# Kernel tuning notes

Measured on AMD Instinct MI355X. Metric: run time of the kernel, lower is better.

## Reference

```python
import jax, jax.numpy as jnp
import numpy as np

N_HEADS = 16
N_EMB = 1024
HEAD_SIZE = 64
BLOCK_SIZE = 2048


def setup_inputs() -> dict:
    key = jax.random.key(0)
    k1, k2, k3, k4, k5 = jax.random.split(key, 5)
    B, T, E, H, D = 4, BLOCK_SIZE, N_EMB, N_HEADS, HEAD_SIZE
    s = 1.0 / np.sqrt(E)
    x = jax.random.normal(k1, (B, T, E), dtype=jnp.float32)
    # Stacked per-head projection weights (Linear with bias=False): [H, E, D]
    Wq = jax.random.normal(k2, (H, E, D), dtype=jnp.float32) * s
    Wk = jax.random.normal(k3, (H, E, D), dtype=jnp.float32) * s
    Wv = jax.random.normal(k4, (H, E, D), dtype=jnp.float32) * s
    Wo = jax.random.normal(k5, (H * D, E), dtype=jnp.float32) * (1.0 / np.sqrt(H * D))
    return {"x": x, "Wq": Wq, "Wk": Wk, "Wv": Wv, "Wo": Wo}


def reference(x, Wq, Wk, Wv, Wo):
    # x: [B,T,E]; Wq/Wk/Wv: [H,E,D]; Wo: [H*D,E]
    B, T, E = x.shape
    H, _, D = Wq.shape
    q = jnp.einsum('bte,hed->bhtd', x, Wq)
    k = jnp.einsum('bte,hed->bhtd', x, Wk)
    v = jnp.einsum('bte,hed->bhtd', x, Wv)
    scores = jnp.einsum('bhtd,bhsd->bhts', q, k) * (D ** -0.5)  # [B,H,T,T]
    causal = jnp.tril(jnp.ones((T, T), dtype=bool))
    scores = jnp.where(causal, scores, -jnp.inf)
    wei = jax.nn.softmax(scores, axis=-1)  # dropout is identity in eval mode
    out = jnp.einsum('bhts,bhsd->bhtd', wei, v)  # [B,H,T,D]
    out = out.transpose(0, 2, 1, 3).reshape(B, T, H * D)  # concat heads
    return out @ Wo  # [B,T,E]
```

## Files before the change

### kernel.cpp

```cpp
#include <hip/hip_runtime.h>

#define B_  4
#define T_  2048
#define E_  1024
#define H_  16
#define D_  64
#define HD_ 1024
#define BT_ 8192

typedef __bf16 bf16x8 __attribute__((ext_vector_type(8)));
typedef float  f32x4  __attribute__((ext_vector_type(4)));

static __device__ __forceinline__ unsigned short f2bf(float f) {
  __bf16 h = (__bf16)f;
  return __builtin_bit_cast(unsigned short, h);
}
static __device__ __forceinline__ bf16x8 ldb8(const unsigned short* p) {
  return *(const bf16x8*)p;
}

#define GLD_LDS16(gp, lp)                                                      \
  __builtin_amdgcn_global_load_lds(                                            \
      (const __attribute__((address_space(1))) void*)(gp),                     \
      (__attribute__((address_space(3))) void*)(lp), 16, 0, 0)

__global__ __launch_bounds__(256) void prep_k(const float* __restrict__ x,
                                              const float* __restrict__ Wq,
                                              const float* __restrict__ Wk,
                                              const float* __restrict__ Wv,
                                              const float* __restrict__ Wo,
                                              unsigned short* __restrict__ xb,
                                              unsigned short* __restrict__ wT,
                                              unsigned short* __restrict__ woT) {
  const int bid = blockIdx.x, tid = threadIdx.x;
  if (bid < 2048) {
    #pragma unroll
    for (int p = 0; p < 4; ++p) {
      int i = bid * 1024 + p * 256 + tid;
      float4 v = ((const float4*)x)[i];
      ushort4 o;
      o.x = f2bf(v.x); o.y = f2bf(v.y); o.z = f2bf(v.z); o.w = f2bf(v.w);
      ((ushort4*)xb)[i] = o;
    }
    return;
  }
  __shared__ float tl[64 * 65];
  if (bid < 2816) {
    const int tix = bid - 2048;
    const int w = tix >> 8;
    const int h = (tix >> 4) & 15;
    const int e0 = (tix & 15) * 64;
    const float* src = (w == 0) ? Wq : (w == 1) ? Wk : Wv;
    #pragma unroll
    for (int rr = 0; rr < 4; ++rr) {
      const int e = e0 + rr * 16 + (tid >> 4);
      const int d4 = (tid & 15) * 4;
      float4 v = *(const float4*)&src[(size_t)(h * 1024 + e) * 64 + d4];
      tl[(e - e0) * 65 + d4 + 0] = v.x;
      tl[(e - e0) * 65 + d4 + 1] = v.y;
      tl[(e - e0) * 65 + d4 + 2] = v.z;
      tl[(e - e0) * 65 + d4 + 3] = v.w;
    }
    __syncthreads();
    #pragma unroll
    for (int cc = 0; cc < 4; ++cc) {
      const int d = cc * 16 + (tid >> 4);
      const int e4 = (tid & 15) * 4;
      ushort4 o;
      o.x = f2bf(tl[(e4 + 0) * 65 + d]);
      o.y = f2bf(tl[(e4 + 1) * 65 + d]);
      o.z = f2bf(tl[(e4 + 2) * 65 + d]);
      o.w = f2bf(tl[(e4 + 3) * 65 + d]);
      *(ushort4*)&wT[(size_t)((w * 16 + h) * 64 + d) * 1024 + e0 + e4] = o;
    }
    return;
  }
  {
    const int tix = bid - 2816;
    const int hd0 = (tix >> 4) * 64;
    const int e0 = (tix & 15) * 64;
    #pragma unroll
    for (int rr = 0; rr < 4; ++rr) {
      const int hd = hd0 + rr * 16 + (tid >> 4);
      const int e4 = (tid & 15) * 4;
      float4 v = *(const float4*)&Wo[(size_t)hd * 1024 + e0 + e4];
      tl[(hd - hd0) * 65 + e4 + 0] = v.x;
      tl[(hd - hd0) * 65 + e4 + 1] = v.y;
      tl[(hd - hd0) * 65 + e4 + 2] = v.z;
      tl[(hd - hd0) * 65 + e4 + 3] = v.w;
    }
    __syncthreads();
    #pragma unroll
    for (int cc = 0; cc < 4; ++cc) {
      const int e = e0 + cc * 16 + (tid >> 4);
      const int hd4 = (tid & 15) * 4;
      ushort4 o;
      o.x = f2bf(tl[(hd4 + 0) * 65 + (e - e0)]);
      o.y = f2bf(tl[(hd4 + 1) * 65 + (e - e0)]);
      o.z = f2bf(tl[(hd4 + 2) * 65 + (e - e0)]);
      o.w = f2bf(tl[(hd4 + 3) * 65 + (e - e0)]);
      *(ushort4*)&woT[(size_t)e * 1024 + hd0 + hd4] = o;
    }
  }
}

static __device__ __forceinline__ void gemm_core(const unsigned short* __restrict__ A,
                                                 const unsigned short* __restrict__ BT,
                                                 const int K, const int m0, const int n0,
                                                 unsigned short* lA, unsigned short* lB,
                                                 f32x4 acc[4][4]) {
  const int tid  = threadIdx.x;
  const int wave = tid >> 6;
  const int lane = tid & 63;
  const int wm = wave & 1, wn = wave >> 1;
  const int l16 = lane & 15, quad = lane >> 4;
  const int nkt = K >> 6;

  const int sr = tid >> 3;
  const int sc = ((tid & 7) ^ (sr & 7)) * 8;
  const int sw = l16 & 7;
  const int sl0 = (quad ^ sw) << 3;
  const int sl1 = ((4 + quad) ^ sw) << 3;

#define STG(kt) do {                                                            \
    const size_t kb = (size_t)(kt) * 64 + sc;                                   \
    unsigned short* dA = lA + ((kt) & 1) * 8192 + wave * 512;                   \
    unsigned short* dB = lB + ((kt) & 1) * 8192 + wave * 512;                   \
    GLD_LDS16(A  + (size_t)(m0 +      sr) * K + kb, dA);                        \
    GLD_LDS16(A  + (size_t)(m0 + 32 + sr) * K + kb, dA + 2048);                 \
    GLD_LDS16(A  + (size_t)(m0 + 64 + sr) * K + kb, dA + 4096);                 \
    GLD_LDS16(A  + (size_t)(m0 + 96 + sr) * K + kb, dA + 6144);                 \
    GLD_LDS16(BT + (size_t)(n0 +      sr) * K + kb, dB);                        \
    GLD_LDS16(BT + (size_t)(n0 + 32 + sr) * K + kb, dB + 2048);                 \
    GLD_LDS16(BT + (size_t)(n0 + 64 + sr) * K + kb, dB + 4096);                 \
    GLD_LDS16(BT + (size_t)(n0 + 96 + sr) * K + kb, dB + 6144);                 \
  } while (0)

  #pragma unroll
  for (int i = 0; i < 4; ++i)
    #pragma unroll
    for (int j = 0; j < 4; ++j) acc[i][j] = (f32x4){0.f, 0.f, 0.f, 0.f};

  STG(0);
  for (int kt = 0; kt < nkt; ++kt) {
    __syncthreads();
    if (kt + 1 < nkt) STG(kt + 1);
    const unsigned short* cA = lA + (kt & 1) * 8192;
    const unsigned short* cB = lB + (kt & 1) * 8192;
    bf16x8 aF[4][2], bF[4][2];
    #pragma unroll
    for (int mi = 0; mi < 4; ++mi) {
      const int ar = (wm * 64 + mi * 16 + l16) * 64;
      aF[mi][0] = ldb8(cA + ar + sl0);
      aF[mi][1] = ldb8(cA + ar + sl1);
    }
    #pragma unroll
    for (int nj = 0; nj < 4; ++nj) {
      const int br = (wn * 64 + nj * 16 + l16) * 64;
      bF[nj][0] = ldb8(cB + br + sl0);
      bF[nj][1] = ldb8(cB + br + sl1);
    }
    __builtin_amdgcn_s_setprio(1);
    #pragma unroll
    for (int mi = 0; mi < 4; ++mi)
      #pragma unroll
      for (int nj = 0; nj < 4; ++nj) {
        acc[mi][nj] = __builtin_amdgcn_mfma_f32_16x16x32_bf16(aF[mi][0], bF[nj][0],
                                                              acc[mi][nj], 0, 0, 0);
        acc[mi][nj] = __builtin_amdgcn_mfma_f32_16x16x32_bf16(aF[mi][1], bF[nj][1],
                                                              acc[mi][nj], 0, 0, 0);
      }
    __builtin_amdgcn_s_setprio(0);
  }
#undef STG
}

__global__ __launch_bounds__(256) void qkv_gemm_k(const unsigned short* __restrict__ xb,
                                                  const unsigned short* __restrict__ wT,
                                                  unsigned short* __restrict__ q,
                                                  unsigned short* __restrict__ k,
                                                  unsigned short* __restrict__ vT) {
  __shared__ unsigned short lA[2 * 128 * 64], lB[2 * 128 * 64];
  f32x4 acc[4][4];
  const int m0 = blockIdx.x * 128, n0 = blockIdx.y * 128;
  gemm_core(xb, wT, E_, m0, n0, lA, lB, acc);

  const int wave = threadIdx.x >> 6, lane = threadIdx.x & 63;
  const int wm = wave & 1, wn = wave >> 1;
  const int l16 = lane & 15, quad = lane >> 4;
  const int type = n0 >> 10;
  const float C = 0.18033688011112042f;
  #pragma unroll
  for (int i = 0; i < 4; ++i) {
    #pragma unroll
    for (int j = 0; j < 4; ++j) {
      const int n = n0 + wn * 64 + j * 16 + l16;
      const int h = (n >> 6) & 15, d = n & 63;
      #pragma unroll
      for (int r = 0; r < 4; ++r) {
        const int m = m0 + wm * 64 + i * 16 + quad * 4 + r;
        const int b = m >> 11, t = m & (T_ - 1);
        if (type == 0)
          q[((size_t)(b * H_ + h) * T_ + t) * D_ + d] = f2bf(acc[i][j][r] * C);
        else if (type == 1)
          k[((size_t)(b * H_ + h) * T_ + t) * D_ + d] = f2bf(acc[i][j][r]);
        else
          vT[((size_t)(b * H_ + h) * D_ + d) * T_ + t] = f2bf(acc[i][j][r]);
      }
    }
  }
}

__global__ __launch_bounds__(256) void proj_k(const unsigned short* __restrict__ ao,
                                              const unsigned short* __restrict__ woT,
                                              float* __restrict__ out) {
  __shared__ unsigned short lA[2 * 128 * 64], lB[2 * 128 * 64];
  f32x4 acc[4][4];
  const int m0 = blockIdx.x * 128, n0 = blockIdx.y * 128;
  gemm_core(ao, woT, HD_, m0, n0, lA, lB, acc);

  const int wave = threadIdx.x >> 6, lane = threadIdx.x & 63;
  const int wm = wave & 1, wn = wave >> 1;
  const int l16 = lane & 15, quad = lane >> 4;
  #pragma unroll
  for (int i = 0; i < 4; ++i)
    #pragma unroll
    for (int j = 0; j < 4; ++j)
      #pragma unroll
      for (int r = 0; r < 4; ++r)
        out[(size_t)(m0 + wm * 64 + i * 16 + quad * 4 + r) * E_ +
            n0 + wn * 64 + j * 16 + l16] = acc[i][j][r];
}

__global__ __launch_bounds__(256) void attn_k(const unsigned short* __restrict__ q,
                                              const unsigned short* __restrict__ k,
                                              const unsigned short* __restrict__ vT,
                                              unsigned short* __restrict__ ao) {
  __shared__ unsigned short lK[2][64 * 64];
  __shared__ unsigned short lV[2][64 * 64];
  __shared__ unsigned short lP[4][32][72];
  const int tid  = threadIdx.x;
  const int lane = tid & 63;
  const int wave = tid >> 6;
  const int l16  = lane & 15;
  const int quad = lane >> 4;
  const int id    = (int)blockIdx.x;
  const int bhid  = id & 63;
  const int qpair = id >> 6;
  const int h = bhid & 15, b = bhid >> 4;
  const size_t bh = (size_t)(b * H_ + h);
  const unsigned short* qp = q  + bh * (T_ * D_);
  const unsigned short* kp = k  + bh * (T_ * D_);
  const unsigned short* vp = vT + bh * (D_ * T_);

  const int srow = tid >> 3;
  const int kseg = (tid & 7) ^ (srow & 7);
  const int sw = (l16 & 7);

  #pragma unroll
  for (int pr = 0; pr < 2; ++pr) {
    const int qblk = (pr == 0) ? qpair : 15 - qpair;
    const int q0 = qblk * 128 + wave * 32;

    bf16x8 aq[2][2];
    #pragma unroll
    for (int rb = 0; rb < 2; ++rb)
      #pragma unroll
      for (int hh = 0; hh < 2; ++hh)
        aq[rb][hh] = ldb8(qp + (q0 + rb * 16 + l16) * D_ + hh * 32 + quad * 8);

    float lr[2][4];
    f32x4 o[2][4];
    #pragma unroll
    for (int rb = 0; rb < 2; ++rb) {
      #pragma unroll
      for (int r = 0; r < 4; ++r) lr[rb][r] = 0.f;
      #pragma unroll
      for (int nb = 0; nb < 4; ++nb) o[rb][nb] = (f32x4){0.f, 0.f, 0.f, 0.f};
    }

    const int nch = 2 * (qblk + 1);

    {
      unsigned short* Kb = lK[0];
      unsigned short* Vb = lV[0];
      GLD_LDS16(kp + srow * D_ + kseg * 8, Kb + wave * 512);
      GLD_LDS16(kp + (32 + srow) * D_ + kseg * 8, Kb + 2048 + wave * 512);
      GLD_LDS16(vp + (size_t)srow * T_ + kseg * 8, Vb + wave * 512);
      GLD_LDS16(vp + (size_t)(32 + srow) * T_ + kseg * 8, Vb + 2048 + wave * 512);
    }

    for (int c = 0; c < nch; ++c) {
      __syncthreads();
      if (c + 1 < nch) {
        const int s1 = (c + 1) * 64;
        unsigned short* Kb = lK[(c + 1) & 1];
        unsigned short* Vb = lV[(c + 1) & 1];
        GLD_LDS16(kp + (s1 + srow) * D_ + kseg * 8, Kb + wave * 512);
        GLD_LDS16(kp + (s1 + 32 + srow) * D_ + kseg * 8, Kb + 2048 + wave * 512);
        GLD_LDS16(vp + (size_t)srow * T_ + s1 + kseg * 8, Vb + wave * 512);
        GLD_LDS16(vp + (size_t)(32 + srow) * T_ + s1 + kseg * 8, Vb + 2048 + wave * 512);
      }
      const int s0 = c * 64;
      const unsigned short* Kb = lK[c & 1];
      const unsigned short* Vb = lV[c & 1];
      f32x4 sc[2][4];
      #pragma unroll
      for (int rb = 0; rb < 2; ++rb)
        #pragma unroll
        for (int j = 0; j < 4; ++j) sc[rb][j] = (f32x4){0.f, 0.f, 0.f, 0.f};
      #pragma unroll
      for (int j = 0; j < 4; ++j) {
        const int sr = j * 16 + l16;
        bf16x8 bk0 = ldb8(Kb + sr * 64 + ((quad ^ sw) << 3));
        bf16x8 bk1 = ldb8(Kb + sr * 64 + (((4 + quad) ^ sw) << 3));
        #pragma unroll
        for (int rb = 0; rb < 2; ++rb) {
          sc[rb][j] = __builtin_amdgcn_mfma_f32_16x16x32_bf16(aq[rb][0], bk0, sc[rb][j], 0, 0, 0);
          sc[rb][j] = __builtin_amdgcn_mfma_f32_16x16x32_bf16(aq[rb][1], bk1, sc[rb][j], 0, 0, 0);
        }
      }
      const bool domask = (c == nch - 1) || (c == nch - 2);
      #pragma unroll
      for (int rb = 0; rb < 2; ++rb) {
        #pragma unroll
        for (int j = 0; j < 4; ++j) {
          #pragma unroll
          for (int r = 0; r < 4; ++r) {
            float p = __builtin_amdgcn_exp2f(sc[rb][j][r]);
            if (domask) {
              const int qg = q0 + rb * 16 + quad * 4 + r;
              if (s0 + j * 16 + l16 > qg) p = 0.f;
            }
            lr[rb][r] += p;
            lP[wave][rb * 16 + quad * 4 + r][j * 16 + l16] = f2bf(p);
          }
        }
      }
      __builtin_amdgcn_wave_barrier();
      bf16x8 aP[2][2];
      #pragma unroll
      for (int rb = 0; rb < 2; ++rb)
        #pragma unroll
        for (int hh = 0; hh < 2; ++hh)
          aP[rb][hh] = ldb8(&lP[wave][rb * 16 + l16][hh * 32 + quad * 8]);
      __builtin_amdgcn_wave_barrier();
      #pragma unroll
      for (int nb = 0; nb < 4; ++nb) {
        const int d = nb * 16 + l16;
        bf16x8 bV0 = ldb8(Vb + d * 64 + ((quad ^ sw) << 3));
        bf16x8 bV1 = ldb8(Vb + d * 64 + (((4 + quad) ^ sw) << 3));
        #pragma unroll
        for (int rb = 0; rb < 2; ++rb) {
          o[rb][nb] = __builtin_amdgcn_mfma_f32_16x16x32_bf16(aP[rb][0], bV0, o[rb][nb], 0, 0, 0);
          o[rb][nb] = __builtin_amdgcn_mfma_f32_16x16x32_bf16(aP[rb][1], bV1, o[rb][nb], 0, 0, 0);
        }
      }
    }

    #pragma unroll
    for (int off = 1; off < 16; off <<= 1)
      #pragma unroll
      for (int rb = 0; rb < 2; ++rb)
        #pragma unroll
        for (int r = 0; r < 4; ++r)
          lr[rb][r] += __shfl_xor(lr[rb][r], off, 64);
    #pragma unroll
    for (int rb = 0; rb < 2; ++rb) {
      #pragma unroll
      for (int r = 0; r < 4; ++r) {
        const float inv = 1.0f / lr[rb][r];
        const int t = q0 + rb * 16 + quad * 4 + r;
        #pragma unroll
        for (int nb = 0; nb < 4; ++nb)
          ao[((size_t)(b * T_ + t) * H_ + h) * D_ + nb * 16 + l16] = f2bf(o[rb][nb][r] * inv);
      }
    }
  }
}


extern "C" void kernel_launch(void* const* d_in, const int* in_sizes, int n_in,
                              void* d_out, int out_size, void* d_ws, size_t ws_size,
                              hipStream_t stream) {
  const float* x  = (const float*)d_in[0];
  const float* Wq = (const float*)d_in[1];
  const float* Wk = (const float*)d_in[2];
  const float* Wv = (const float*)d_in[3];
  const float* Wo = (const float*)d_in[4];
  float* out = (float*)d_out;

  char* ws = (char*)d_ws;
  unsigned short* xb   = (unsigned short*)(ws + 0);
  unsigned short* wT   = (unsigned short*)(ws + 16777216);
  unsigned short* woT  = (unsigned short*)(ws + 23068672);
  unsigned short* qb   = (unsigned short*)(ws + 25165824);
  unsigned short* kb   = (unsigned short*)(ws + 41943040);
  unsigned short* vTb  = (unsigned short*)(ws + 58720256);
  unsigned short* aob  = (unsigned short*)(ws + 75497472);

  prep_k<<<dim3(3072), dim3(256), 0, stream>>>(x, Wq, Wk, Wv, Wo, xb, wT, woT);
  qkv_gemm_k<<<dim3(BT_ / 128, 3072 / 128), dim3(256), 0, stream>>>(xb, wT, qb, kb, vTb);
  attn_k<<<dim3(512), dim3(256), 0, stream>>>(qb, kb, vTb, aob);
  proj_k<<<dim3(BT_ / 128, E_ / 128), dim3(256), 0, stream>>>(aob, woT, out);
}
```

Measured before the change: 252.8 us.

## Use triple-buffered K=32 pipeline with vmcnt waits for QKV GEMM

Adds a new GEMM core for the QKV projection that uses K-tiles of 32 with three LDS buffers, issuing loads two iterations ahead. Explicit vmcnt waits plus raw barriers replace the full __syncthreads. The goal is to hide global-to-LDS latency better and shrink LDS usage from 64KB to 48KB, which may allow higher occupancy. In exchange it doubles the number of loop iterations and barriers per K. The output projection keeps the original double-buffered K=64 core.

```diff
diff --git a/kernel.cpp b/kernel.cpp
--- a/kernel.cpp
+++ b/kernel.cpp
@@ -104,11 +104,80 @@
   }
 }
 
-static __device__ __forceinline__ void gemm_core(const unsigned short* __restrict__ A,
-                                                 const unsigned short* __restrict__ BT,
-                                                 const int K, const int m0, const int n0,
-                                                 unsigned short* lA, unsigned short* lB,
-                                                 f32x4 acc[4][4]) {
+static __device__ __forceinline__ void gemm_core32(const unsigned short* __restrict__ A,
+                                                   const unsigned short* __restrict__ BT,
+                                                   const int K, const int m0, const int n0,
+                                                   unsigned short* lA, unsigned short* lB,
+                                                   f32x4 acc[4][4]) {
+  const int tid  = threadIdx.x;
+  const int wave = tid >> 6;
+  const int lane = tid & 63;
+  const int wm = wave & 1, wn = wave >> 1;
+  const int l16 = lane & 15, quad = lane >> 4;
+  const int nit = K >> 5;
+
+  const int sr = tid >> 2;
+  const int sc = ((tid & 3) ^ ((sr >> 1) & 3)) * 8;
+  const int slot = (quad ^ ((l16 >> 1) & 3)) << 3;
+
+#define STG32(kt, bi) do {                                                      \
+    const size_t kb = (size_t)(kt) * 32 + sc;                                   \
+    unsigned short* dA = lA + (bi) * 4096 + wave * 512;                         \
+    unsigned short* dB = lB + (bi) * 4096 + wave * 512;                         \
+    GLD_LDS16(A  + (size_t)(m0 +      sr) * K + kb, dA);                        \
+    GLD_LDS16(A  + (size_t)(m0 + 64 + sr) * K + kb, dA + 2048);                 \
+    GLD_LDS16(BT + (size_t)(n0 +      sr) * K + kb, dB);                        \
+    GLD_LDS16(BT + (size_t)(n0 + 64 + sr) * K + kb, dB + 2048);                 \
+  } while (0)
+
+  #pragma unroll
+  for (int i = 0; i < 4; ++i)
+    #pragma unroll
+    for (int j = 0; j < 4; ++j) acc[i][j] = (f32x4){0.f, 0.f, 0.f, 0.f};
+
+  STG32(0, 0);
+  STG32(1, 1);
+  asm volatile("s_waitcnt vmcnt(4)" ::: "memory");
+  __builtin_amdgcn_s_barrier();
+
+  int cb = 0, sb = 2;
+  for (int it = 0; it < nit; ++it) {
+    if (it + 2 < nit) STG32(it + 2, sb);
+    const unsigned short* cA = lA + cb * 4096;
+    const unsigned short* cB = lB + cb * 4096;
+    bf16x8 aF[4], bF[4];
+    #pragma unroll
+    for (int mi = 0; mi < 4; ++mi)
+      aF[mi] = ldb8(cA + (wm * 64 + mi * 16 + l16) * 32 + slot);
+    #pragma unroll
+    for (int nj = 0; nj < 4; ++nj)
+      bF[nj] = ldb8(cB + (wn * 64 + nj * 16 + l16) * 32 + slot);
+    __builtin_amdgcn_s_setprio(1);
+    #pragma unroll
+    for (int mi = 0; mi < 4; ++mi)
+      #pragma unroll
+      for (int nj = 0; nj < 4; ++nj)
+        acc[mi][nj] = __builtin_amdgcn_mfma_f32_16x16x32_bf16(aF[mi], bF[nj],
+                                                              acc[mi][nj], 0, 0, 0);
+    __builtin_amdgcn_s_setprio(0);
+    if (it + 1 < nit) {
+      if (it + 2 < nit)
+        asm volatile("s_waitcnt vmcnt(4)" ::: "memory");
+      else
+        asm volatile("s_waitcnt vmcnt(0)" ::: "memory");
+      __builtin_amdgcn_s_barrier();
+    }
+    cb = (cb == 2) ? 0 : cb + 1;
+    sb = (sb == 2) ? 0 : sb + 1;
+  }
+#undef STG32
+}
+
+static __device__ __forceinline__ void gemm_core64(const unsigned short* __restrict__ A,
+                                                   const unsigned short* __restrict__ BT,
+                                                   const int K, const int m0, const int n0,
+                                                   unsigned short* lA, unsigned short* lB,
+                                                   f32x4 acc[4][4]) {
   const int tid  = threadIdx.x;
   const int wave = tid >> 6;
   const int lane = tid & 63;
@@ -122,7 +191,7 @@
   const int sl0 = (quad ^ sw) << 3;
   const int sl1 = ((4 + quad) ^ sw) << 3;
 
-#define STG(kt) do {                                                            \
+#define STG64(kt) do {                                                          \
     const size_t kb = (size_t)(kt) * 64 + sc;                                   \
     unsigned short* dA = lA + ((kt) & 1) * 8192 + wave * 512;                   \
     unsigned short* dB = lB + ((kt) & 1) * 8192 + wave * 512;                   \
@@ -141,10 +210,10 @@
     #pragma unroll
     for (int j = 0; j < 4; ++j) acc[i][j] = (f32x4){0.f, 0.f, 0.f, 0.f};
 
-  STG(0);
+  STG64(0);
   for (int kt = 0; kt < nkt; ++kt) {
     __syncthreads();
-    if (kt + 1 < nkt) STG(kt + 1);
+    if (kt + 1 < nkt) STG64(kt + 1);
     const unsigned short* cA = lA + (kt & 1) * 8192;
     const unsigned short* cB = lB + (kt & 1) * 8192;
     bf16x8 aF[4][2], bF[4][2];
@@ -172,7 +241,7 @@
       }
     __builtin_amdgcn_s_setprio(0);
   }
-#undef STG
+#undef STG64
 }
 
 __global__ __launch_bounds__(256) void qkv_gemm_k(const unsigned short* __restrict__ xb,
@@ -180,10 +249,10 @@
                                                   unsigned short* __restrict__ q,
                                                   unsigned short* __restrict__ k,
                                                   unsigned short* __restrict__ vT) {
-  __shared__ unsigned short lA[2 * 128 * 64], lB[2 * 128 * 64];
+  __shared__ unsigned short lA[3 * 128 * 32], lB[3 * 128 * 32];
   f32x4 acc[4][4];
   const int m0 = blockIdx.x * 128, n0 = blockIdx.y * 128;
-  gemm_core(xb, wT, E_, m0, n0, lA, lB, acc);
+  gemm_core32(xb, wT, E_, m0, n0, lA, lB, acc);
 
   const int wave = threadIdx.x >> 6, lane = threadIdx.x & 63;
   const int wm = wave & 1, wn = wave >> 1;
@@ -217,7 +286,7 @@
   __shared__ unsigned short lA[2 * 128 * 64], lB[2 * 128 * 64];
   f32x4 acc[4][4];
   const int m0 = blockIdx.x * 128, n0 = blockIdx.y * 128;
-  gemm_core(ao, woT, HD_, m0, n0, lA, lB, acc);
+  gemm_core64(ao, woT, HD_, m0, n0, lA, lB, acc);
 
   const int wave = threadIdx.x >> 6, lane = threadIdx.x & 63;
   const int wm = wave & 1, wn = wave >> 1;
```

Measured after the change: 260.4 us. +3.0%, slower.
